# Performance work log

Measured on AMD Instinct MI355X. Metric: run time of the kernel, lower is better.

The kernel has to match this reference:

```python
import jax, jax.numpy as jnp
import numpy as np

EMB = 512
HEADS = 8
WINDOW = 128


def setup_inputs() -> dict:
    key = jax.random.key(0)
    ks = jax.random.split(key, 9)
    s = 1.0 / np.sqrt(EMB)
    x = jax.random.normal(ks[0], (2, 4096, EMB), dtype=jnp.float32)
    mk = lambda k: jax.random.uniform(k, (EMB, EMB), jnp.float32, -s, s)
    mb = lambda k: jax.random.uniform(k, (EMB,), jnp.float32, -s, s)
    return {
        "x": x,
        "Wq": mk(ks[1]), "bq": mb(ks[2]),
        "Wk": mk(ks[3]), "bk": mb(ks[4]),
        "Wv": mk(ks[5]), "bv": mb(ks[6]),
        "Wo": mk(ks[7]), "bo": mb(ks[8]),
    }


def _split_heads(y, b, n):
    # [b, n, emb] -> [b, h, n, d]
    return y.reshape(b, n, HEADS, EMB // HEADS).transpose(0, 2, 1, 3)


def reference(x, Wq, bq, Wk, bk, Wv, bv, Wo, bo):
    b, n, _ = x.shape
    q = _split_heads(x @ Wq.T + bq, b, n)
    k = _split_heads(x @ Wk.T + bk, b, n)
    v = _split_heads(x @ Wv.T + bv, b, n)
    energy = jnp.einsum('bhqd,bhkd->bhqk', q, k)  # [b,h,n,n]
    idx = jnp.arange(n)
    # banded mask: disallowed where |i - j| > window (matches torch loop)
    disallow = jnp.abs(idx[:, None] - idx[None, :]) > WINDOW
    fmin = jnp.float32(np.finfo(np.float32).min)
    energy = jnp.where(disallow[None, None], fmin, energy)
    att = jax.nn.softmax(energy / jnp.float32(np.sqrt(EMB)), axis=-1)
    out = jnp.einsum('bhql,bhld->bhqd', att, v)
    out = out.transpose(0, 2, 1, 3).reshape(b, n, EMB)
    return out @ Wo.T + bo
```

## Files before the change

kernel.cpp:

```cpp
#include <hip/hip_runtime.h>

#define EMB 512
#define HEADS 8
#define HD 64
#define NSEQ 4096
#define BATCH 2
#define WINDOW 128

typedef unsigned short u16;
typedef __attribute__((ext_vector_type(8))) short bf16x8;
typedef __attribute__((ext_vector_type(4))) float f32x4;

#define XS 4194304u
#define WS 262144u
#define BS 512u

__device__ __forceinline__ float bf2f(u16 u) {
    union { unsigned int i; float f; } x;
    x.i = ((unsigned int)u) << 16;
    return x.f;
}

__device__ __forceinline__ u16 f2bf(float f) {
    union { float f; unsigned int i; } x;
    x.f = f;
    unsigned int i = x.i;
    unsigned int lsb = (i >> 16) & 1u;
    i += 0x7fffu + lsb;
    return (u16)(i >> 16);
}

struct raw8 { uint4 lo, hi; };

__device__ __forceinline__ raw8 loadraw8(const void* base, size_t off, int isbf) {
    raw8 r;
    if (isbf) {
        r.lo = *(const uint4*)((const u16*)base + off);
    } else {
        const float* f = (const float*)base + off;
        r.lo = *(const uint4*)f;
        r.hi = *(const uint4*)(f + 4);
    }
    return r;
}

__device__ __forceinline__ uint4 cvt8(const raw8& r, int isbf) {
    if (isbf) return r.lo;
    const float* a = (const float*)&r.lo;
    const float* b = (const float*)&r.hi;
    uint4 o;
    o.x = (unsigned)f2bf(a[0]) | ((unsigned)f2bf(a[1]) << 16);
    o.y = (unsigned)f2bf(a[2]) | ((unsigned)f2bf(a[3]) << 16);
    o.z = (unsigned)f2bf(b[0]) | ((unsigned)f2bf(b[1]) << 16);
    o.w = (unsigned)f2bf(b[2]) | ((unsigned)f2bf(b[3]) << 16);
    return o;
}

__device__ __forceinline__ int probe_bf16(const void* p) {
    const int lane = threadIdx.x & 63;
    u16 w = ((const u16*)p)[lane * 2];
    int e = (w >> 7) & 0xff;
    bool sane = (w == 0) || (e >= 100 && e <= 140);
    unsigned long long m = __ballot(sane);
    return __popcll(m) >= 48;
}

__global__ __launch_bounds__(256)
void prepass(const void* __restrict__ x,
             const void* __restrict__ Wq, const void* __restrict__ bq,
             const void* __restrict__ Wk, const void* __restrict__ bk,
             const void* __restrict__ Wv, const void* __restrict__ bv,
             const void* __restrict__ Wo, const void* __restrict__ bo,
             u16* __restrict__ xb, u16* __restrict__ wb, u16* __restrict__ bb,
             int* __restrict__ flags)
{
    const int fx  = probe_bf16(x);
    const int fwq = probe_bf16(Wq), fbq = probe_bf16(bq);
    const int fwk = probe_bf16(Wk), fbk = probe_bf16(bk);
    const int fwv = probe_bf16(Wv), fbv = probe_bf16(bv);
    const int fwo = probe_bf16(Wo), fbo = probe_bf16(bo);
    if (blockIdx.x == 0 && threadIdx.x == 0) flags[0] = fx;

    size_t idx = ((size_t)blockIdx.x * 256 + threadIdx.x) * 8;
    const size_t T_X = XS, T_W = XS + 4 * (size_t)WS, T_ALL = T_W + 4 * (size_t)BS;
    if (idx >= T_ALL) return;

    const void* src; int fl; u16* dst; size_t off;
    if (idx < T_X) {
        src = x; fl = fx; dst = xb; off = idx;
    } else if (idx < T_W) {
        size_t w = idx - T_X;
        int wi = (int)(w / WS); off = w % WS;
        src = (wi == 0) ? Wq : (wi == 1) ? Wk : (wi == 2) ? Wv : Wo;
        fl  = (wi == 0) ? fwq : (wi == 1) ? fwk : (wi == 2) ? fwv : fwo;
        dst = wb + (size_t)wi * WS;
    } else {
        size_t b = idx - T_W;
        int bi = (int)(b / BS); off = b % BS;
        src = (bi == 0) ? bq : (bi == 1) ? bk : (bi == 2) ? bv : bo;
        fl  = (bi == 0) ? fbq : (bi == 1) ? fbk : (bi == 2) ? fbv : fbo;
        dst = bb + (size_t)bi * BS;
    }
    *(uint4*)(dst + off) = cvt8(loadraw8(src, off, fl), fl);
}

__global__ __launch_bounds__(256)
void qkv_gemm(const u16* __restrict__ X, const u16* __restrict__ Wall,
              const u16* __restrict__ ball,
              u16* __restrict__ qo, u16* __restrict__ ko, u16* __restrict__ vo)
{
    __shared__ __align__(16) u16 As[128 * 32];
    __shared__ __align__(16) u16 Bs[128 * 32];

    const int tid  = threadIdx.x;
    const int wave = tid >> 6;
    const int lane = tid & 63;
    const int quad = lane >> 4;
    const int l16  = lane & 15;
    const int wm = wave >> 1, wn = wave & 1;

    const int m0 = blockIdx.x * 128;
    const int by = blockIdx.y;
    const int wsel = by >> 2;
    const int n0 = (by & 3) * 128;

    const u16* W  = Wall + (size_t)wsel * WS;
    const u16* bi = ball + (size_t)wsel * BS;
    u16* out      = (wsel == 0) ? qo : (wsel == 1) ? ko : vo;
    const float oscale = (wsel == 0) ? 0.04419417382415922f : 1.0f;

    f32x4 acc[4][4];
#pragma unroll
    for (int i = 0; i < 4; ++i)
#pragma unroll
        for (int j = 0; j < 4; ++j)
            acc[i][j] = (f32x4){0.f, 0.f, 0.f, 0.f};

    const int c1 = tid, c2 = tid + 256;
    const int r1 = c1 >> 2, k1 = (c1 & 3) * 8;
    const int r2 = c2 >> 2, k2 = (c2 & 3) * 8;

    uint4 a1 = *(const uint4*)(X + (size_t)(m0 + r1) * EMB + k1);
    uint4 a2 = *(const uint4*)(X + (size_t)(m0 + r2) * EMB + k2);
    uint4 b1 = *(const uint4*)(W + (size_t)(n0 + r1) * EMB + k1);
    uint4 b2 = *(const uint4*)(W + (size_t)(n0 + r2) * EMB + k2);

    for (int kt = 0; kt < 16; ++kt) {
        __syncthreads();
        *(uint4*)&As[c1 * 8] = a1;
        *(uint4*)&As[c2 * 8] = a2;
        *(uint4*)&Bs[c1 * 8] = b1;
        *(uint4*)&Bs[c2 * 8] = b2;
        __syncthreads();

        if (kt < 15) {
            const int kk0 = (kt + 1) * 32;
            a1 = *(const uint4*)(X + (size_t)(m0 + r1) * EMB + kk0 + k1);
            a2 = *(const uint4*)(X + (size_t)(m0 + r2) * EMB + kk0 + k2);
            b1 = *(const uint4*)(W + (size_t)(n0 + r1) * EMB + kk0 + k1);
            b2 = *(const uint4*)(W + (size_t)(n0 + r2) * EMB + kk0 + k2);
        }

        bf16x8 af[4], bfr[4];
#pragma unroll
        for (int i = 0; i < 4; ++i)
            af[i] = *(const bf16x8*)&As[(wm * 64 + i * 16 + l16) * 32 + quad * 8];
#pragma unroll
        for (int j = 0; j < 4; ++j)
            bfr[j] = *(const bf16x8*)&Bs[(wn * 64 + j * 16 + l16) * 32 + quad * 8];
#pragma unroll
        for (int i = 0; i < 4; ++i)
#pragma unroll
            for (int j = 0; j < 4; ++j)
                acc[i][j] = __builtin_amdgcn_mfma_f32_16x16x32_bf16(af[i], bfr[j], acc[i][j], 0, 0, 0);
    }

#pragma unroll
    for (int j = 0; j < 4; ++j) {
        const int col = n0 + wn * 64 + j * 16 + l16;
        const float bv_ = bf2f(bi[col]);
        const int h = col >> 6, d = col & 63;
#pragma unroll
        for (int i = 0; i < 4; ++i) {
#pragma unroll
            for (int r = 0; r < 4; ++r) {
                const int row = m0 + wm * 64 + i * 16 + quad * 4 + r;
                const int b = row >> 12, n = row & 4095;
                out[(((size_t)(b * HEADS + h) * NSEQ) + n) * HD + d] =
                    f2bf((acc[i][j][r] + bv_) * oscale);
            }
        }
    }
}

#define KP 72
__global__ __launch_bounds__(256)
void attn_mfma(const u16* __restrict__ q, const u16* __restrict__ k,
               const u16* __restrict__ v, u16* __restrict__ ao)
{
    __shared__ __align__(16) u16 Ks[64 * KP];
    __shared__ __align__(16) u16 Vt[64 * KP];
    __shared__ __align__(16) u16 Pb[4][16 * KP];

    const int tid  = threadIdx.x;
    const int wave = tid >> 6;
    const int lane = tid & 63;
    const int quad = lane >> 4;
    const int l16  = lane & 15;

    const int bh = blockIdx.y;
    const int q0 = blockIdx.x * 64;
    const int qw = q0 + wave * 16;
    const size_t base = (size_t)bh * NSEQ * HD;

    bf16x8 qa0 = *(const bf16x8*)(q + base + (size_t)(qw + l16) * HD + quad * 8);
    bf16x8 qa1 = *(const bf16x8*)(q + base + (size_t)(qw + l16) * HD + 32 + quad * 8);

    f32x4 O[4];
    float m_run[4], l_run[4];
#pragma unroll
    for (int t = 0; t < 4; ++t) O[t] = (f32x4){0.f, 0.f, 0.f, 0.f};
#pragma unroll
    for (int r = 0; r < 4; ++r) { m_run[r] = -1e30f; l_run[r] = 0.f; }

    const int key_s[2] = { tid >> 3, (tid + 256) >> 3 };
    const int ch8      = (tid & 7) * 8;

    uint4 pkv[2], pvv[2];
#pragma unroll
    for (int s = 0; s < 2; ++s) {
        int kg = q0 - 128 + key_s[s];
        kg = (kg < 0) ? 0 : (kg > NSEQ - 1 ? NSEQ - 1 : kg);
        const size_t goff = base + (size_t)kg * HD + ch8;
        pkv[s] = *(const uint4*)(k + goff);
        pvv[s] = *(const uint4*)(v + goff);
    }

    for (int c = 0; c < 5; ++c) {
        const int kbase = q0 - 128 + c * 64;

        __syncthreads();
#pragma unroll
        for (int s = 0; s < 2; ++s) {
            const int key = key_s[s], d0 = ch8;
            *(uint4*)&Ks[key * KP + d0] = pkv[s];
            uint4 vv = pvv[s];
            u16 e[8];
            e[0] = (u16)(vv.x & 0xffff); e[1] = (u16)(vv.x >> 16);
            e[2] = (u16)(vv.y & 0xffff); e[3] = (u16)(vv.y >> 16);
            e[4] = (u16)(vv.z & 0xffff); e[5] = (u16)(vv.z >> 16);
            e[6] = (u16)(vv.w & 0xffff); e[7] = (u16)(vv.w >> 16);
#pragma unroll
            for (int j = 0; j < 8; ++j)
                Vt[(d0 + j) * KP + key] = e[j];
        }
        __syncthreads();

        if (c < 4) {
#pragma unroll
            for (int s = 0; s < 2; ++s) {
                int kg = kbase + 64 + key_s[s];
                kg = (kg < 0) ? 0 : (kg > NSEQ - 1 ? NSEQ - 1 : kg);
                const size_t goff = base + (size_t)kg * HD + ch8;
                pkv[s] = *(const uint4*)(k + goff);
                pvv[s] = *(const uint4*)(v + goff);
            }
        }

        f32x4 sv[4];
#pragma unroll
        for (int t = 0; t < 4; ++t) {
            bf16x8 b0 = *(const bf16x8*)&Ks[(t * 16 + l16) * KP + quad * 8];
            bf16x8 b1 = *(const bf16x8*)&Ks[(t * 16 + l16) * KP + 32 + quad * 8];
            f32x4 sacc = (f32x4){0.f, 0.f, 0.f, 0.f};
            sacc = __builtin_amdgcn_mfma_f32_16x16x32_bf16(qa0, b0, sacc, 0, 0, 0);
            sacc = __builtin_amdgcn_mfma_f32_16x16x32_bf16(qa1, b1, sacc, 0, 0, 0);
            sv[t] = sacc;
        }

#pragma unroll
        for (int t = 0; t < 4; ++t) {
            const int jg = kbase + t * 16 + l16;
            const bool jok = ((unsigned)jg) < (unsigned)NSEQ;
#pragma unroll
            for (int r = 0; r < 4; ++r) {
                const int iq = qw + quad * 4 + r;
                const bool band = ((unsigned)(iq - jg + WINDOW)) <= (unsigned)(2 * WINDOW);
                if (!(jok && band)) sv[t][r] = -1e30f;
            }
        }

        float mnew[4];
#pragma unroll
        for (int r = 0; r < 4; ++r)
            mnew[r] = fmaxf(fmaxf(sv[0][r], sv[1][r]), fmaxf(sv[2][r], sv[3][r]));
#pragma unroll
        for (int off = 1; off < 16; off <<= 1)
#pragma unroll
            for (int r = 0; r < 4; ++r)
                mnew[r] = fmaxf(mnew[r], __shfl_xor(mnew[r], off, 64));

        float alpha[4], mi[4];
#pragma unroll
        for (int r = 0; r < 4; ++r) {
            mi[r] = fmaxf(m_run[r], mnew[r]);
            alpha[r] = __expf(m_run[r] - mi[r]);
            m_run[r] = mi[r];
        }

        float p[4][4], lnew[4] = {0.f, 0.f, 0.f, 0.f};
#pragma unroll
        for (int t = 0; t < 4; ++t)
#pragma unroll
            for (int r = 0; r < 4; ++r) {
                float pv = (sv[t][r] > -1e29f) ? __expf(sv[t][r] - mi[r]) : 0.f;
                p[t][r] = pv;
                lnew[r] += pv;
            }
#pragma unroll
        for (int off = 1; off < 16; off <<= 1)
#pragma unroll
            for (int r = 0; r < 4; ++r)
                lnew[r] += __shfl_xor(lnew[r], off, 64);
#pragma unroll
        for (int r = 0; r < 4; ++r)
            l_run[r] = l_run[r] * alpha[r] + lnew[r];

#pragma unroll
        for (int t = 0; t < 4; ++t)
#pragma unroll
            for (int r = 0; r < 4; ++r)
                O[t][r] *= alpha[r];

#pragma unroll
        for (int t = 0; t < 4; ++t)
#pragma unroll
            for (int r = 0; r < 4; ++r)
                Pb[wave][(quad * 4 + r) * KP + t * 16 + l16] = f2bf(p[t][r]);

#pragma unroll
        for (int ks = 0; ks < 2; ++ks) {
            bf16x8 pa = *(const bf16x8*)&Pb[wave][l16 * KP + ks * 32 + quad * 8];
#pragma unroll
            for (int t = 0; t < 4; ++t) {
                bf16x8 vb = *(const bf16x8*)&Vt[(t * 16 + l16) * KP + ks * 32 + quad * 8];
                O[t] = __builtin_amdgcn_mfma_f32_16x16x32_bf16(pa, vb, O[t], 0, 0, 0);
            }
        }
    }

    const int bb = bh >> 3, hh = bh & 7;
    float rl[4];
#pragma unroll
    for (int r = 0; r < 4; ++r) rl[r] = 1.f / l_run[r];
#pragma unroll
    for (int t = 0; t < 4; ++t)
#pragma unroll
        for (int r = 0; r < 4; ++r) {
            const int iq = qw + quad * 4 + r;
            ao[((size_t)(bb * NSEQ + iq)) * EMB + hh * HD + t * 16 + l16] =
                f2bf(O[t][r] * rl[r]);
        }
}

__global__ __launch_bounds__(256)
void out_gemm(const u16* __restrict__ A, const u16* __restrict__ W,
              const u16* __restrict__ bias, void* __restrict__ out,
              const int* __restrict__ flags)
{
    __shared__ __align__(16) u16 As[128 * 32];
    __shared__ __align__(16) u16 Bs[128 * 32];

    const int tid  = threadIdx.x;
    const int wave = tid >> 6;
    const int lane = tid & 63;
    const int quad = lane >> 4;
    const int l16  = lane & 15;
    const int wm = wave >> 1, wn = wave & 1;

    const int m0 = blockIdx.x * 128;
    const int n0 = blockIdx.y * 128;
    const int fo = flags[0];

    f32x4 acc[4][4];
#pragma unroll
    for (int i = 0; i < 4; ++i)
#pragma unroll
        for (int j = 0; j < 4; ++j)
            acc[i][j] = (f32x4){0.f, 0.f, 0.f, 0.f};

    const int c1 = tid, c2 = tid + 256;
    const int r1 = c1 >> 2, k1 = (c1 & 3) * 8;
    const int r2 = c2 >> 2, k2 = (c2 & 3) * 8;

    uint4 a1 = *(const uint4*)(A + (size_t)(m0 + r1) * EMB + k1);
    uint4 a2 = *(const uint4*)(A + (size_t)(m0 + r2) * EMB + k2);
    uint4 b1 = *(const uint4*)(W + (size_t)(n0 + r1) * EMB + k1);
    uint4 b2 = *(const uint4*)(W + (size_t)(n0 + r2) * EMB + k2);

    for (int kt = 0; kt < 16; ++kt) {
        __syncthreads();
        *(uint4*)&As[c1 * 8] = a1;
        *(uint4*)&As[c2 * 8] = a2;
        *(uint4*)&Bs[c1 * 8] = b1;
        *(uint4*)&Bs[c2 * 8] = b2;
        __syncthreads();

        if (kt < 15) {
            const int kk0 = (kt + 1) * 32;
            a1 = *(const uint4*)(A + (size_t)(m0 + r1) * EMB + kk0 + k1);
            a2 = *(const uint4*)(A + (size_t)(m0 + r2) * EMB + kk0 + k2);
            b1 = *(const uint4*)(W + (size_t)(n0 + r1) * EMB + kk0 + k1);
            b2 = *(const uint4*)(W + (size_t)(n0 + r2) * EMB + kk0 + k2);
        }

        bf16x8 af[4], bfr[4];
#pragma unroll
        for (int i = 0; i < 4; ++i)
            af[i] = *(const bf16x8*)&As[(wm * 64 + i * 16 + l16) * 32 + quad * 8];
#pragma unroll
        for (int j = 0; j < 4; ++j)
            bfr[j] = *(const bf16x8*)&Bs[(wn * 64 + j * 16 + l16) * 32 + quad * 8];
#pragma unroll
        for (int i = 0; i < 4; ++i)
#pragma unroll
            for (int j = 0; j < 4; ++j)
                acc[i][j] = __builtin_amdgcn_mfma_f32_16x16x32_bf16(af[i], bfr[j], acc[i][j], 0, 0, 0);
    }

#pragma unroll
    for (int j = 0; j < 4; ++j) {
        const int col = n0 + wn * 64 + j * 16 + l16;
        const float bv_ = bf2f(bias[col]);
#pragma unroll
        for (int i = 0; i < 4; ++i) {
#pragma unroll
            for (int r = 0; r < 4; ++r) {
                const int row = m0 + wm * 64 + i * 16 + quad * 4 + r;
                const float val = acc[i][j][r] + bv_;
                const size_t idx = (size_t)row * EMB + col;
                if (fo) ((u16*)out)[idx] = f2bf(val);
                else    ((float*)out)[idx] = val;
            }
        }
    }
}

extern "C" void kernel_launch(void* const* d_in, const int* in_sizes, int n_in,
                              void* d_out, int out_size, void* d_ws, size_t ws_size,
                              hipStream_t stream)
{
    const size_t HSZ  = (size_t)BATCH * HEADS * NSEQ * HD;
    char* base = (char*)d_ws;
    int* flags = (int*)base;
    const size_t off = 256;

    u16* xb = (u16*)(base + off);
    u16* wb = xb + XS;
    u16* bb = wb + 4 * (size_t)WS;
    u16* kk = bb + 4 * (size_t)BS;
    u16* vv = kk + HSZ;
    u16* ao = vv + HSZ;
    u16* qq = ao + HSZ;

    const size_t need_t1 = off + 2 * (XS + 4 * (size_t)WS + 4 * (size_t)BS + 4 * HSZ);
    if (ws_size < need_t1) {
        qq = (u16*)d_out;
    }

    prepass<<<dim3(2561), 256, 0, stream>>>(d_in[0], d_in[1], d_in[2], d_in[3],
                                            d_in[4], d_in[5], d_in[6], d_in[7],
                                            d_in[8], xb, wb, bb, flags);
    qkv_gemm<<<dim3(64, 12), 256, 0, stream>>>(xb, wb, bb, qq, kk, vv);
    attn_mfma<<<dim3(64, 16), 256, 0, stream>>>(qq, kk, vv, ao);
    out_gemm<<<dim3(64, 4), 256, 0, stream>>>(ao, wb + 3 * (size_t)WS, bb + 3 * (size_t)BS,
                                              d_out, flags);
}
```

Before: 151.7 us.

## Store V transposed from projection and compute softmax denominator via ones-row MFMA

```diff
diff --git a/kernel.cpp b/kernel.cpp
--- a/kernel.cpp
+++ b/kernel.cpp
@@ -175,31 +175,52 @@
                 acc[i][j] = __builtin_amdgcn_mfma_f32_16x16x32_bf16(af[i], bfr[j], acc[i][j], 0, 0, 0);
     }
 
-#pragma unroll
-    for (int j = 0; j < 4; ++j) {
-        const int col = n0 + wn * 64 + j * 16 + l16;
-        const float bv_ = bf2f(bi[col]);
-        const int h = col >> 6, d = col & 63;
-#pragma unroll
-        for (int i = 0; i < 4; ++i) {
-#pragma unroll
-            for (int r = 0; r < 4; ++r) {
-                const int row = m0 + wm * 64 + i * 16 + quad * 4 + r;
-                const int b = row >> 12, n = row & 4095;
-                out[(((size_t)(b * HEADS + h) * NSEQ) + n) * HD + d] =
-                    f2bf((acc[i][j][r] + bv_) * oscale);
+    if (wsel != 2) {
+#pragma unroll
+        for (int j = 0; j < 4; ++j) {
+            const int col = n0 + wn * 64 + j * 16 + l16;
+            const float bv_ = bf2f(bi[col]);
+            const int h = col >> 6, d = col & 63;
+#pragma unroll
+            for (int i = 0; i < 4; ++i) {
+#pragma unroll
+                for (int r = 0; r < 4; ++r) {
+                    const int row = m0 + wm * 64 + i * 16 + quad * 4 + r;
+                    const int b = row >> 12, n = row & 4095;
+                    out[(((size_t)(b * HEADS + h) * NSEQ) + n) * HD + d] =
+                        f2bf((acc[i][j][r] + bv_) * oscale);
+                }
+            }
+        }
+    } else {
+#pragma unroll
+        for (int j = 0; j < 4; ++j) {
+            const int col = n0 + wn * 64 + j * 16 + l16;
+            const float bv_ = bf2f(bi[col]);
+            const int h = col >> 6, d = col & 63;
+#pragma unroll
+            for (int i = 0; i < 4; ++i) {
+                const int row0 = m0 + wm * 64 + i * 16 + quad * 4;
+                const int b = row0 >> 12, n = row0 & 4095;
+                uint2 pk;
+                pk.x = (unsigned)f2bf(acc[i][j][0] + bv_) |
+                       ((unsigned)f2bf(acc[i][j][1] + bv_) << 16);
+                pk.y = (unsigned)f2bf(acc[i][j][2] + bv_) |
+                       ((unsigned)f2bf(acc[i][j][3] + bv_) << 16);
+                *(uint2*)(out + ((size_t)(b * HEADS + h) * HD + d) * NSEQ + n) = pk;
             }
         }
     }
 }
 
 #define KP 72
+#define VP 72
 __global__ __launch_bounds__(256)
 void attn_mfma(const u16* __restrict__ q, const u16* __restrict__ k,
-               const u16* __restrict__ v, u16* __restrict__ ao)
+               const u16* __restrict__ vt, u16* __restrict__ ao)
 {
     __shared__ __align__(16) u16 Ks[64 * KP];
-    __shared__ __align__(16) u16 Vt[64 * KP];
+    __shared__ __align__(16) u16 Vt[80 * VP];
     __shared__ __align__(16) u16 Pb[4][16 * KP];
 
     const int tid  = threadIdx.x;
@@ -208,32 +229,46 @@
     const int quad = lane >> 4;
     const int l16  = lane & 15;
 
-    const int bh = blockIdx.y;
-    const int q0 = blockIdx.x * 64;
+    int wg = blockIdx.y * 64 + blockIdx.x;
+    wg = (wg & 7) * 128 + (wg >> 3);
+    const int bh = wg >> 6;
+    const int q0 = (wg & 63) * 64;
+
     const int qw = q0 + wave * 16;
     const size_t base = (size_t)bh * NSEQ * HD;
+    const bool interior = (q0 >= 128) && (q0 <= NSEQ - 192);
+
+    if (tid < VP) {
+        Vt[64 * VP + tid] = (u16)0x3f80;
+#pragma unroll
+        for (int rr = 65; rr < 80; ++rr) Vt[rr * VP + tid] = 0;
+    }
 
     bf16x8 qa0 = *(const bf16x8*)(q + base + (size_t)(qw + l16) * HD + quad * 8);
     bf16x8 qa1 = *(const bf16x8*)(q + base + (size_t)(qw + l16) * HD + 32 + quad * 8);
 
-    f32x4 O[4];
-    float m_run[4], l_run[4];
+    f32x4 O[4], O4;
+    float m_run[4];
 #pragma unroll
     for (int t = 0; t < 4; ++t) O[t] = (f32x4){0.f, 0.f, 0.f, 0.f};
-#pragma unroll
-    for (int r = 0; r < 4; ++r) { m_run[r] = -1e30f; l_run[r] = 0.f; }
+    O4 = (f32x4){0.f, 0.f, 0.f, 0.f};
+#pragma unroll
+    for (int r = 0; r < 4; ++r) m_run[r] = -1e30f;
 
     const int key_s[2] = { tid >> 3, (tid + 256) >> 3 };
     const int ch8      = (tid & 7) * 8;
+
+    const int pacol = (quad * 8) ^ ((l16 >> 2) << 4);
 
     uint4 pkv[2], pvv[2];
 #pragma unroll
     for (int s = 0; s < 2; ++s) {
         int kg = q0 - 128 + key_s[s];
         kg = (kg < 0) ? 0 : (kg > NSEQ - 1 ? NSEQ - 1 : kg);
-        const size_t goff = base + (size_t)kg * HD + ch8;
-        pkv[s] = *(const uint4*)(k + goff);
-        pvv[s] = *(const uint4*)(v + goff);
+        pkv[s] = *(const uint4*)(k + base + (size_t)kg * HD + ch8);
+        int kc = q0 - 128 + ch8;
+        kc = (kc < 0) ? 0 : (kc > NSEQ - 8 ? NSEQ - 8 : kc);
+        pvv[s] = *(const uint4*)(vt + base + (size_t)key_s[s] * NSEQ + kc);
     }
 
     for (int c = 0; c < 5; ++c) {
@@ -242,17 +277,8 @@
         __syncthreads();
 #pragma unroll
         for (int s = 0; s < 2; ++s) {
-            const int key = key_s[s], d0 = ch8;
-            *(uint4*)&Ks[key * KP + d0] = pkv[s];
-            uint4 vv = pvv[s];
-            u16 e[8];
-            e[0] = (u16)(vv.x & 0xffff); e[1] = (u16)(vv.x >> 16);
-            e[2] = (u16)(vv.y & 0xffff); e[3] = (u16)(vv.y >> 16);
-            e[4] = (u16)(vv.z & 0xffff); e[5] = (u16)(vv.z >> 16);
-            e[6] = (u16)(vv.w & 0xffff); e[7] = (u16)(vv.w >> 16);
-#pragma unroll
-            for (int j = 0; j < 8; ++j)
-                Vt[(d0 + j) * KP + key] = e[j];
+            *(uint4*)&Ks[key_s[s] * KP + ch8] = pkv[s];
+            *(uint4*)&Vt[key_s[s] * VP + ch8] = pvv[s];
         }
         __syncthreads();
 
@@ -261,33 +287,38 @@
             for (int s = 0; s < 2; ++s) {
                 int kg = kbase + 64 + key_s[s];
                 kg = (kg < 0) ? 0 : (kg > NSEQ - 1 ? NSEQ - 1 : kg);
-                const size_t goff = base + (size_t)kg * HD + ch8;
-                pkv[s] = *(const uint4*)(k + goff);
-                pvv[s] = *(const uint4*)(v + goff);
-            }
-        }
-
+                pkv[s] = *(const uint4*)(k + base + (size_t)kg * HD + ch8);
+                int kc = kbase + 64 + ch8;
+                kc = (kc < 0) ? 0 : (kc > NSEQ - 8 ? NSEQ - 8 : kc);
+                pvv[s] = *(const uint4*)(vt + base + (size_t)key_s[s] * NSEQ + kc);
+            }
+        }
+
+        const int dkb = kbase - qw;
         f32x4 sv[4];
 #pragma unroll
         for (int t = 0; t < 4; ++t) {
+            const int dk = dkb + t * 16;
+            if (dk < -143 || dk > 143) {
+                sv[t] = (f32x4){-1e30f, -1e30f, -1e30f, -1e30f};
+                continue;
+            }
             bf16x8 b0 = *(const bf16x8*)&Ks[(t * 16 + l16) * KP + quad * 8];
             bf16x8 b1 = *(const bf16x8*)&Ks[(t * 16 + l16) * KP + 32 + quad * 8];
             f32x4 sacc = (f32x4){0.f, 0.f, 0.f, 0.f};
             sacc = __builtin_amdgcn_mfma_f32_16x16x32_bf16(qa0, b0, sacc, 0, 0, 0);
             sacc = __builtin_amdgcn_mfma_f32_16x16x32_bf16(qa1, b1, sacc, 0, 0, 0);
+            if (!interior || dk < -113 || dk > 113) {
+                const int jg = kbase + t * 16 + l16;
+                const bool jok = ((unsigned)jg) < (unsigned)NSEQ;
+#pragma unroll
+                for (int r = 0; r < 4; ++r) {
+                    const int iq = qw + quad * 4 + r;
+                    const bool band = ((unsigned)(iq - jg + WINDOW)) <= (unsigned)(2 * WINDOW);
+                    if (!(jok && band)) sacc[r] = -1e30f;
+                }
+            }
             sv[t] = sacc;
-        }
-
-#pragma unroll
-        for (int t = 0; t < 4; ++t) {
-            const int jg = kbase + t * 16 + l16;
-            const bool jok = ((unsigned)jg) < (unsigned)NSEQ;
-#pragma unroll
-            for (int r = 0; r < 4; ++r) {
-                const int iq = qw + quad * 4 + r;
-                const bool band = ((unsigned)(iq - jg + WINDOW)) <= (unsigned)(2 * WINDOW);
-                if (!(jok && band)) sv[t][r] = -1e30f;
-            }
         }
 
         float mnew[4];
@@ -308,51 +339,45 @@
             m_run[r] = mi[r];
         }
 
-        float p[4][4], lnew[4] = {0.f, 0.f, 0.f, 0.f};
-#pragma unroll
-        for (int t = 0; t < 4; ++t)
-#pragma unroll
-            for (int r = 0; r < 4; ++r) {
-                float pv = (sv[t][r] > -1e29f) ? __expf(sv[t][r] - mi[r]) : 0.f;
-                p[t][r] = pv;
-                lnew[r] += pv;
-            }
-#pragma unroll
-        for (int off = 1; off < 16; off <<= 1)
-#pragma unroll
-            for (int r = 0; r < 4; ++r)
-                lnew[r] += __shfl_xor(lnew[r], off, 64);
-#pragma unroll
-        for (int r = 0; r < 4; ++r)
-            l_run[r] = l_run[r] * alpha[r] + lnew[r];
-
 #pragma unroll
         for (int t = 0; t < 4; ++t)
 #pragma unroll
             for (int r = 0; r < 4; ++r)
                 O[t][r] *= alpha[r];
-
-#pragma unroll
-        for (int t = 0; t < 4; ++t)
-#pragma unroll
-            for (int r = 0; r < 4; ++r)
-                Pb[wave][(quad * 4 + r) * KP + t * 16 + l16] = f2bf(p[t][r]);
-
-#pragma unroll
-        for (int ks = 0; ks < 2; ++ks) {
-            bf16x8 pa = *(const bf16x8*)&Pb[wave][l16 * KP + ks * 32 + quad * 8];
+#pragma unroll
+        for (int r = 0; r < 4; ++r)
+            O4[r] *= alpha[r];
+
+#pragma unroll
+        for (int t = 0; t < 4; ++t) {
+            const int tc = (t ^ quad) * 16 + l16;
+#pragma unroll
+            for (int r = 0; r < 4; ++r) {
+                const float pv = (sv[t][r] > -1e29f) ? __expf(sv[t][r] - mi[r]) : 0.f;
+                Pb[wave][(quad * 4 + r) * KP + tc] = f2bf(pv);
+            }
+        }
+
+#pragma unroll
+        for (int ks2 = 0; ks2 < 2; ++ks2) {
+            bf16x8 pa = *(const bf16x8*)&Pb[wave][l16 * KP + (pacol ^ (ks2 * 32))];
 #pragma unroll
             for (int t = 0; t < 4; ++t) {
-                bf16x8 vb = *(const bf16x8*)&Vt[(t * 16 + l16) * KP + ks * 32 + quad * 8];
+                bf16x8 vb = *(const bf16x8*)&Vt[(t * 16 + l16) * VP + ks2 * 32 + quad * 8];
                 O[t] = __builtin_amdgcn_mfma_f32_16x16x32_bf16(pa, vb, O[t], 0, 0, 0);
             }
+            bf16x8 vb4 = *(const bf16x8*)&Vt[(64 + l16) * VP + ks2 * 32 + quad * 8];
+            O4 = __builtin_amdgcn_mfma_f32_16x16x32_bf16(pa, vb4, O4, 0, 0, 0);
         }
     }
 
     const int bb = bh >> 3, hh = bh & 7;
     float rl[4];
 #pragma unroll
-    for (int r = 0; r < 4; ++r) rl[r] = 1.f / l_run[r];
+    for (int r = 0; r < 4; ++r) {
+        const float ls = __shfl(O4[r], lane & 48, 64);
+        rl[r] = 1.f / ls;
+    }
 #pragma unroll
     for (int t = 0; t < 4; ++t)
 #pragma unroll
```

Result: slower. 163.4 us (+7.7%).
